# Kernel tuning notes

Hardware: AMD Instinct MI355X
Metric: run time of the kernel (lower is better)

## Reference

```python
import math
import jax, jax.numpy as jnp
import numpy as np

B, S, T = 32, 512, 180
D, F, L, H = 512, 2048, 6, 8
DH = D // H


def _pos_encoding(length, d):
    pos = np.arange(length, dtype=np.float32)[:, None]
    div = np.exp(np.arange(0, d, 2, dtype=np.float32) * (-math.log(10000.0) / d))
    pe = np.zeros((length, d), dtype=np.float32)
    pe[:, 0::2] = np.sin(pos * div)
    pe[:, 1::2] = np.cos(pos * div)
    return jnp.asarray(pe)


def _ln(x, scale, bias):
    mu = x.mean(-1, keepdims=True)
    var = ((x - mu) ** 2).mean(-1, keepdims=True)
    return (x - mu) * jax.lax.rsqrt(var + 1e-5) * scale + bias


def _mha(q_in, kv_in, w, b, causal=False):
    # w: [4, D, D] = (Wq, Wk, Wv, Wo); b: [4, D]
    b_, sq = q_in.shape[:2]
    q = (q_in @ w[0] + b[0]).reshape(b_, sq, H, DH)
    k = (kv_in @ w[1] + b[1]).reshape(b_, -1, H, DH)
    v = (kv_in @ w[2] + b[2]).reshape(b_, -1, H, DH)
    s = jnp.einsum('bqhd,bkhd->bhqk', q, k) / math.sqrt(DH)
    if causal:
        mask = jnp.tril(jnp.ones((sq, k.shape[1]), dtype=bool))
        s = jnp.where(mask, s, -1e9)
    a = jax.nn.softmax(s, axis=-1)
    o = jnp.einsum('bhqk,bkhd->bqhd', a, v).reshape(b_, sq, D)
    return o @ w[3] + b[3]


def _ffn(x, w1, b1, w2, b2):
    return jax.nn.relu(x @ w1 + b1) @ w2 + b2


def setup_inputs() -> dict:
    key = jax.random.key(0)
    ks = jax.random.split(key, 16)
    n = lambda k, shape: jax.random.normal(k, shape, jnp.float32) * 0.02
    return {
        'x': jax.random.normal(ks[0], (B, S, 2), jnp.float32),
        'y_cv_teacher': jax.random.normal(ks[1], (B, T, 1), jnp.float32),
        'src_proj_w': n(ks[2], (2, D)), 'src_proj_b': jnp.zeros((D,), jnp.float32),
        'tgt_proj_w': n(ks[3], (1, D)), 'tgt_proj_b': jnp.zeros((D,), jnp.float32),
        'enc_attn_w': n(ks[4], (L, 4, D, D)), 'enc_attn_b': jnp.zeros((L, 4, D), jnp.float32),
        'enc_ffn_w1': n(ks[5], (L, D, F)), 'enc_ffn_b1': jnp.zeros((L, F), jnp.float32),
        'enc_ffn_w2': n(ks[6], (L, F, D)), 'enc_ffn_b2': jnp.zeros((L, D), jnp.float32),
        'enc_ln_scale': jnp.ones((L, 2, D), jnp.float32), 'enc_ln_bias': jnp.zeros((L, 2, D), jnp.float32),
        'dec_self_w': n(ks[7], (L, 4, D, D)), 'dec_self_b': jnp.zeros((L, 4, D), jnp.float32),
        'dec_cross_w': n(ks[8], (L, 4, D, D)), 'dec_cross_b': jnp.zeros((L, 4, D), jnp.float32),
        'dec_ffn_w1': n(ks[9], (L, D, F)), 'dec_ffn_b1': jnp.zeros((L, F), jnp.float32),
        'dec_ffn_w2': n(ks[10], (L, F, D)), 'dec_ffn_b2': jnp.zeros((L, D), jnp.float32),
        'dec_ln_scale': jnp.ones((L, 3, D), jnp.float32), 'dec_ln_bias': jnp.zeros((L, 3, D), jnp.float32),
        'out_w': n(ks[11], (D, 1)), 'out_b': jnp.zeros((1,), jnp.float32),
    }


def reference(x, y_cv_teacher, src_proj_w, src_proj_b, tgt_proj_w, tgt_proj_b,
              enc_attn_w, enc_attn_b, enc_ffn_w1, enc_ffn_b1, enc_ffn_w2, enc_ffn_b2,
              enc_ln_scale, enc_ln_bias, dec_self_w, dec_self_b, dec_cross_w, dec_cross_b,
              dec_ffn_w1, dec_ffn_b1, dec_ffn_w2, dec_ffn_b2, dec_ln_scale, dec_ln_bias,
              out_w, out_b):
    pe = _pos_encoding(512, D)
    # encoder (post-norm, relu FFN, dropout disabled = eval semantics)
    h = x @ src_proj_w + src_proj_b + pe[: x.shape[1]]
    for i in range(L):
        h = _ln(h + _mha(h, h, enc_attn_w[i], enc_attn_b[i]), enc_ln_scale[i, 0], enc_ln_bias[i, 0])
        h = _ln(h + _ffn(h, enc_ffn_w1[i], enc_ffn_b1[i], enc_ffn_w2[i], enc_ffn_b2[i]),
                enc_ln_scale[i, 1], enc_ln_bias[i, 1])
    memory = h
    # teacher-forced decoder input: [start=0, y_cv_teacher[:-1]]
    tgt_in = jnp.concatenate([jnp.zeros((x.shape[0], 1, 1), x.dtype), y_cv_teacher[:, :-1, :]], axis=1)
    d = tgt_in @ tgt_proj_w + tgt_proj_b + pe[: tgt_in.shape[1]]
    for i in range(L):
        d = _ln(d + _mha(d, d, dec_self_w[i], dec_self_b[i], causal=True),
                dec_ln_scale[i, 0], dec_ln_bias[i, 0])
        d = _ln(d + _mha(d, memory, dec_cross_w[i], dec_cross_b[i]),
                dec_ln_scale[i, 1], dec_ln_bias[i, 1])
        d = _ln(d + _ffn(d, dec_ffn_w1[i], dec_ffn_b1[i], dec_ffn_w2[i], dec_ffn_b2[i]),
                dec_ln_scale[i, 2], dec_ln_bias[i, 2])
    return d @ out_w + out_b  # [B, T, 1]
```

## Files before the change

kernel.cpp:

```cpp
#include <hip/hip_runtime.h>
#include <math.h>

#define B_  32
#define S_  512
#define T_  180
#define D_  512
#define F_  2048
#define L_  6
#define H_  8
#define DH_ 64

typedef unsigned short u16;
typedef __attribute__((ext_vector_type(8))) short short8;
typedef __attribute__((ext_vector_type(4))) float floatx4;

__device__ __forceinline__ float bf2f(u16 h) {
    union { unsigned u; float f; } un; un.u = ((unsigned)h) << 16; return un.f;
}
__device__ __forceinline__ u16 f2bf(float f) {
    union { float f; unsigned u; } un; un.f = f;
    unsigned u = un.u;
    u += 0x7fffu + ((u >> 16) & 1u);
    return (u16)(u >> 16);
}

__device__ __forceinline__ void gload16(const u16* g, u16* l) {
    __builtin_amdgcn_global_load_lds(
        (const __attribute__((address_space(1))) void*)g,
        (__attribute__((address_space(3))) void*)l, 16, 0, 0);
}

__device__ __forceinline__ float pos_enc(int pos, int c) {
    int i2 = c & ~1;
    float div = expf(-(float)i2 * (9.210340371976184f / 512.0f));
    float arg = (float)pos * div;
    return (c & 1) ? cosf(arg) : sinf(arg);
}

__global__ __launch_bounds__(256) void embed_src_kernel(
    const float* __restrict__ x, const float* __restrict__ w,
    const float* __restrict__ b, u16* __restrict__ h)
{
    int idx = blockIdx.x * 256 + threadIdx.x;
    if (idx >= B_ * S_ * D_) return;
    int c  = idx & (D_ - 1);
    int bs = idx >> 9;
    int s  = bs & (S_ - 1);
    float x0 = x[bs * 2 + 0];
    float x1 = x[bs * 2 + 1];
    h[idx] = f2bf(x0 * w[c] + x1 * w[D_ + c] + b[c] + pos_enc(s, c));
}

__global__ __launch_bounds__(256) void embed_tgt_kernel(
    const float* __restrict__ y, const float* __restrict__ w,
    const float* __restrict__ b, u16* __restrict__ d)
{
    int idx = blockIdx.x * 256 + threadIdx.x;
    if (idx >= B_ * T_ * D_) return;
    int c  = idx & (D_ - 1);
    int bt = idx >> 9;
    int t  = bt % T_;
    int bb = bt / T_;
    float tv = (t == 0) ? 0.0f : y[bb * T_ + (t - 1)];
    d[idx] = f2bf(tv * w[c] + b[c] + pos_enc(t, c));
}

__global__ __launch_bounds__(256) void wconv_kernel(
    const float* __restrict__ W, u16* __restrict__ Wt, int K, int N)
{
    __shared__ float tile[32][33];
    size_t mat = (size_t)blockIdx.z * K * N;
    const float* Wm = W + mat;
    u16* Wtm = Wt + mat;
    int n0 = blockIdx.x * 32, k0 = blockIdx.y * 32;
    int tx = threadIdx.x & 31, ty = threadIdx.x >> 5;
#pragma unroll
    for (int i = 0; i < 32; i += 8)
        tile[ty + i][tx] = Wm[(size_t)(k0 + ty + i) * N + n0 + tx];
    __syncthreads();
#pragma unroll
    for (int i = 0; i < 32; i += 8)
        Wtm[(size_t)(n0 + ty + i) * K + k0 + tx] = f2bf(tile[tx][ty + i]);
}

__global__ __launch_bounds__(256) void gemm_bf16_kernel(
    const u16* __restrict__ A, int lda, const u16* __restrict__ Bt,
    const float* __restrict__ bias, u16* __restrict__ C, int ldc,
    int M, int N, int K, int relu)
{
    __shared__ u16 smem[18432];
    u16* As = smem;
    u16* Bs = smem + 8192;

    int tid  = threadIdx.x;
    int w    = tid >> 6;
    int lane = tid & 63;
    int m0 = blockIdx.y << 7, n0 = blockIdx.x << 7;

    int sr = w * 32 + (lane >> 2);
    int sk = (lane & 3) * 8;
    const u16* ag0 = A  + (size_t)(m0 + sr)      * lda + sk;
    const u16* ag1 = A  + (size_t)(m0 + sr + 16) * lda + sk;
    const u16* bg0 = Bt + (size_t)(n0 + sr)      * K + sk;
    const u16* bg1 = Bt + (size_t)(n0 + sr + 16) * K + sk;
    u16* al0 = As + (w * 2 + 0) * 512;
    u16* al1 = As + (w * 2 + 1) * 512;
    u16* bl0 = Bs + (w * 2 + 0) * 512;
    u16* bl1 = Bs + (w * 2 + 1) * 512;

    int wm = (w >> 1) * 64, wn = (w & 1) * 64;
    int fr = lane & 15;
    int fk = (lane >> 4) * 8;

    floatx4 acc[4][4] = {};

    for (int k0 = 0; k0 < K; k0 += 64) {
#pragma unroll
        for (int hh = 0; hh < 2; ++hh) {
            int go = k0 + hh * 32;
            int lo = hh * 4096;
            gload16(ag0 + go, al0 + lo);
            gload16(ag1 + go, al1 + lo);
            gload16(bg0 + go, bl0 + lo);
            gload16(bg1 + go, bl1 + lo);
        }
        __syncthreads();

#pragma unroll
        for (int hh = 0; hh < 2; ++hh) {
            int lo = hh * 4096;
            short8 af[4], bf[4];
#pragma unroll
            for (int i = 0; i < 4; ++i)
                af[i] = *(const short8*)&As[lo + (wm + i * 16 + fr) * 32 + fk];
#pragma unroll
            for (int j = 0; j < 4; ++j)
                bf[j] = *(const short8*)&Bs[lo + (wn + j * 16 + fr) * 32 + fk];
#pragma unroll
            for (int i = 0; i < 4; ++i)
#pragma unroll
                for (int j = 0; j < 4; ++j)
                    acc[i][j] = __builtin_amdgcn_mfma_f32_16x16x32_bf16(
                        af[i], bf[j], acc[i][j], 0, 0, 0);
        }
        __syncthreads();
    }

    u16* epi = smem + w * 4608;
    int cc = lane & 15;
    int rq = (lane >> 4) * 4;
#pragma unroll
    for (int j = 0; j < 4; ++j) {
        float bj = bias[n0 + wn + j * 16 + cc];
#pragma unroll
        for (int i = 0; i < 4; ++i) {
#pragma unroll
            for (int r = 0; r < 4; ++r) {
                float vv = acc[i][j][r] + bj;
                if (relu) vv = fmaxf(vv, 0.f);
                epi[(i * 16 + rq + r) * 72 + j * 16 + cc] = f2bf(vv);
            }
        }
    }
    __syncthreads();
#pragma unroll
    for (int t = 0; t < 8; ++t) {
        int er = t * 8 + (lane >> 3);
        int ec = (lane & 7) * 8;
        short8 vv = *(const short8*)&epi[er * 72 + ec];
        *(short8*)&C[(size_t)(m0 + wm + er) * ldc + n0 + wn + ec] = vv;
    }
}

#define CEXP 0.1803368801111244f

__global__ __launch_bounds__(256) void attn_mfma_kernel(
    const u16* Q, int qs, const u16* __restrict__ K, int ks,
    const u16* __restrict__ V, u16* O,
    int Sq, int Sk, int causal)
{
    __shared__ u16 Qs[64 * 72];
    __shared__ u16 Ks[64 * 72];
    __shared__ u16 Vt[64 * 72];
    __shared__ u16 Ps[4][16 * 72];

    int tid  = threadIdx.x;
    int w    = tid >> 6;
    int lane = tid & 63;
    int n    = lane & 15;
    int quad = lane >> 4;
    int bh = blockIdx.x;
    int bb = bh >> 3, hhd = bh & 7;
    int q0 = blockIdx.y * 64;

    const u16* Qb = Q + (size_t)bb * Sq * qs + hhd * DH_;
    const u16* Kb = K + (size_t)bb * Sk * ks + hhd * DH_;
    const u16* Vb = V + (size_t)bb * Sk * ks + hhd * DH_;

#pragma unroll
    for (int it = 0; it < 2; ++it) {
        int idx = it * 256 + tid;
        int r = idx >> 3, dg = (idx & 7) * 8;
        int qg = q0 + r;
        short8 vv = {};
        if (qg < Sq) vv = *(const short8*)&Qb[(size_t)qg * qs + dg];
        *(short8*)&Qs[r * 72 + dg] = vv;
    }

    float m_i[4], l_i[4];
    floatx4 o_acc[4] = {};
#pragma unroll
    for (int r = 0; r < 4; ++r) { m_i[r] = -1e30f; l_i[r] = 0.f; }

    int qrow0 = q0 + w * 16 + quad * 4;
    int kend = causal ? ((Sk < q0 + 64) ? Sk : (q0 + 64)) : Sk;
    __syncthreads();

    for (int k0 = 0; k0 < kend; k0 += 64) {
#pragma unroll
        for (int it = 0; it < 2; ++it) {
            int idx = it * 256 + tid;
            int r = idx >> 3, dg = (idx & 7) * 8;
            int kg = k0 + r;
            short8 kv = {}, vv = {};
            if (kg < Sk) {
                kv = *(const short8*)&Kb[(size_t)kg * ks + dg];
                vv = *(const short8*)&Vb[(size_t)kg * ks + dg];
            }
            *(short8*)&Ks[r * 72 + dg] = kv;
            int col = (r + dg) & 63;
#pragma unroll
            for (int j = 0; j < 8; ++j)
                Vt[(dg + j) * 72 + col] = (u16)vv[j];
        }
        __syncthreads();

        floatx4 sc[4] = {};
        short8 aq0 = *(const short8*)&Qs[(w * 16 + n) * 72 + quad * 8];
        short8 aq1 = *(const short8*)&Qs[(w * 16 + n) * 72 + 32 + quad * 8];
#pragma unroll
        for (int j = 0; j < 4; ++j) {
            short8 bk0 = *(const short8*)&Ks[(j * 16 + n) * 72 + quad * 8];
            short8 bk1 = *(const short8*)&Ks[(j * 16 + n) * 72 + 32 + quad * 8];
            sc[j] = __builtin_amdgcn_mfma_f32_16x16x32_bf16(aq0, bk0, sc[j], 0, 0, 0);
            sc[j] = __builtin_amdgcn_mfma_f32_16x16x32_bf16(aq1, bk1, sc[j], 0, 0, 0);
        }

        bool need_mask = (k0 + 64 > Sk) ||
                         (causal && (k0 + 63 > q0 + w * 16));
        if (need_mask) {
#pragma unroll
            for (int j = 0; j < 4; ++j) {
                int kg = k0 + j * 16 + n;
#pragma unroll
                for (int r = 0; r < 4; ++r) {
                    if (kg >= Sk || (causal && kg > qrow0 + r))
                        sc[j][r] = -1e30f;
                }
            }
        }

#pragma unroll
        for (int r = 0; r < 4; ++r) {
            float mx = fmaxf(fmaxf(sc[0][r], sc[1][r]), fmaxf(sc[2][r], sc[3][r]));
#pragma unroll
            for (int off = 8; off > 0; off >>= 1)
                mx = fmaxf(mx, __shfl_xor(mx, off, 16));
            float mnew = fmaxf(m_i[r], mx);
            float alpha = exp2f((m_i[r] - mnew) * CEXP);
            m_i[r] = mnew;
            float ps = 0.f;
#pragma unroll
            for (int j = 0; j < 4; ++j) {
                float p = exp2f((sc[j][r] - mnew) * CEXP);
                sc[j][r] = p; ps += p;
            }
#pragma unroll
            for (int off = 8; off > 0; off >>= 1)
                ps += __shfl_xor(ps, off, 16);
            l_i[r] = l_i[r] * alpha + ps;
#pragma unroll
            for (int jb = 0; jb < 4; ++jb) o_acc[jb][r] *= alpha;
        }

#pragma unroll
        for (int j = 0; j < 4; ++j)
#pragma unroll
            for (int r = 0; r < 4; ++r)
                Ps[w][(quad * 4 + r) * 72 + j * 16 + n] = f2bf(sc[j][r]);

        short8 ap0 = *(const short8*)&Ps[w][n * 72 + quad * 8];
        short8 ap1 = *(const short8*)&Ps[w][n * 72 + 32 + quad * 8];
#pragma unroll
        for (int jb = 0; jb < 4; ++jb) {
            int d = jb * 16 + n;
            int rot = d & ~7;
            short8 bv0 = *(const short8*)&Vt[d * 72 + ((quad * 8 + rot) & 63)];
            short8 bv1 = *(const short8*)&Vt[d * 72 + ((32 + quad * 8 + rot) & 63)];
            o_acc[jb] = __builtin_amdgcn_mfma_f32_16x16x32_bf16(ap0, bv0, o_acc[jb], 0, 0, 0);
            o_acc[jb] = __builtin_amdgcn_mfma_f32_16x16x32_bf16(ap1, bv1, o_acc[jb], 0, 0, 0);
        }
        __syncthreads();
    }

    float inv[4];
#pragma unroll
    for (int r = 0; r < 4; ++r) inv[r] = 1.0f / l_i[r];
    u16* Ob = O + (size_t)bb * Sq * qs + hhd * DH_;
#pragma unroll
    for (int r = 0; r < 4; ++r) {
        int qg = qrow0 + r;
        if (qg < Sq) {
#pragma unroll
            for (int jb = 0; jb < 4; ++jb)
                Ob[(size_t)qg * qs + jb * 16 + n] = f2bf(o_acc[jb][r] * inv[r]);
        }
    }
}

__global__ __launch_bounds__(128) void add_ln_kernel(
    u16* __restrict__ h, const u16* __restrict__ delta,
    const float* __restrict__ scale, const float* __restrict__ bias)
{
    __shared__ float red[2][2];
    int row = blockIdx.x, tid = threadIdx.x;
    int lane = tid & 63, wv = tid >> 6;
    size_t base = (size_t)row * D_ + tid * 4;
    uint2 hv = *(const uint2*)&h[base];
    uint2 dv = *(const uint2*)&delta[base];
    float v0 = bf2f(hv.x & 0xffff) + bf2f(dv.x & 0xffff);
    float v1 = bf2f(hv.x >> 16)    + bf2f(dv.x >> 16);
    float v2 = bf2f(hv.y & 0xffff) + bf2f(dv.y & 0xffff);
    float v3 = bf2f(hv.y >> 16)    + bf2f(dv.y >> 16);

    float a  = v0 + v1 + v2 + v3;
    float b2 = v0 * v0 + v1 * v1 + v2 * v2 + v3 * v3;
#pragma unroll
    for (int off = 32; off > 0; off >>= 1) {
        a  += __shfl_xor(a, off);
        b2 += __shfl_xor(b2, off);
    }
    if (lane == 0) { red[wv][0] = a; red[wv][1] = b2; }
    __syncthreads();
    float S1 = red[0][0] + red[1][0];
    float S2 = red[0][1] + red[1][1];
    float mu = S1 * (1.0f / 512.0f);
    float var = S2 * (1.0f / 512.0f) - mu * mu;
    float rs = rsqrtf(var + 1e-5f);

    int c = tid * 4;
    float4 sc = *(const float4*)&scale[c];
    float4 bi = *(const float4*)&bias[c];
    unsigned lo = (unsigned)f2bf((v0 - mu) * rs * sc.x + bi.x) |
                  ((unsigned)f2bf((v1 - mu) * rs * sc.y + bi.y) << 16);
    unsigned hi = (unsigned)f2bf((v2 - mu) * rs * sc.z + bi.z) |
                  ((unsigned)f2bf((v3 - mu) * rs * sc.w + bi.w) << 16);
    *(uint2*)&h[base] = make_uint2(lo, hi);
}

__global__ __launch_bounds__(64) void out_proj_kernel(
    const u16* __restrict__ d, const float* __restrict__ w,
    const float* __restrict__ b, float* __restrict__ out)
{
    int row = blockIdx.x, lane = threadIdx.x;
    float s = 0.f;
    for (int c = lane; c < D_; c += 64) s += bf2f(d[(size_t)row * D_ + c]) * w[c];
#pragma unroll
    for (int off = 32; off > 0; off >>= 1) s += __shfl_down(s, off);
    if (lane == 0) out[row] = s + b[0];
}

extern "C" void kernel_launch(void* const* d_in, const int* in_sizes, int n_in,
                              void* d_out, int out_size, void* d_ws, size_t ws_size,
                              hipStream_t stream)
{
    const float* x          = (const float*)d_in[0];
    const float* y          = (const float*)d_in[1];
    const float* src_w      = (const float*)d_in[2];
    const float* src_b      = (const float*)d_in[3];
    const float* tgt_w      = (const float*)d_in[4];
    const float* tgt_b      = (const float*)d_in[5];
    const float* enc_attn_w = (const float*)d_in[6];
    const float* enc_attn_b = (const float*)d_in[7];
    const float* enc_ffn_w1 = (const float*)d_in[8];
    const float* enc_ffn_b1 = (const float*)d_in[9];
    const float* enc_ffn_w2 = (const float*)d_in[10];
    const float* enc_ffn_b2 = (const float*)d_in[11];
    const float* enc_ln_s   = (const float*)d_in[12];
    const float* enc_ln_b   = (const float*)d_in[13];
    const float* dec_self_w = (const float*)d_in[14];
    const float* dec_self_b = (const float*)d_in[15];
    const float* dec_cross_w= (const float*)d_in[16];
    const float* dec_cross_b= (const float*)d_in[17];
    const float* dec_ffn_w1 = (const float*)d_in[18];
    const float* dec_ffn_b1 = (const float*)d_in[19];
    const float* dec_ffn_w2 = (const float*)d_in[20];
    const float* dec_ffn_b2 = (const float*)d_in[21];
    const float* dec_ln_s   = (const float*)d_in[22];
    const float* dec_ln_b   = (const float*)d_in[23];
    const float* out_w      = (const float*)d_in[24];
    const float* out_b      = (const float*)d_in[25];
    float* out = (float*)d_out;

    const size_t E_BSD = (size_t)B_ * S_ * D_;
    const size_t E_BTD = (size_t)B_ * T_ * D_;
    const size_t WDD   = (size_t)D_ * D_;
    const size_t WDF   = (size_t)D_ * F_;
    const int MS = B_ * S_;
    const int MT = B_ * T_;

    u16* h    = (u16*)d_ws;
    u16* qkv  = h + E_BSD;
    u16* o    = qkv + (size_t)MS * 1536;
    u16* dbuf = o + E_BSD;
    u16* wsc  = dbuf + E_BTD;
    u16* mid  = qkv;
    u16* cq   = qkv;
    u16* ckv  = qkv + 4 * 1024 * 1024;

    auto gemm = [&](const u16* A, int lda, const u16* Wt, const float* bi,
                    u16* C, int ldc, int M, int N, int K, int relu) {
        dim3 g(N / 128, M / 128);
        gemm_bf16_kernel<<<g, dim3(256), 0, stream>>>(A, lda, Wt, bi, C, ldc,
                                                      M, N, K, relu);
    };
    auto attn = [&](const u16* Qp, int qs, const u16* Kp, int ks,
                    const u16* Vp, u16* Op, int Sq, int Sk, int causal) {
        dim3 g(B_ * H_, (Sq + 63) / 64);
        attn_mfma_kernel<<<g, dim3(256), 0, stream>>>(Qp, qs, Kp, ks, Vp, Op,
                                                      Sq, Sk, causal);
    };
    auto addln = [&](u16* hp, const u16* dp, const float* sc, const float* bi,
                     int rows) {
        add_ln_kernel<<<dim3(rows), dim3(128), 0, stream>>>(hp, dp, sc, bi);
    };
    auto wconv = [&](const float* W, u16* Wt, int K, int N, int nmat) {
        wconv_kernel<<<dim3(N / 32, K / 32, nmat), dim3(256), 0, stream>>>(W, Wt, K, N);
    };

    embed_src_kernel<<<dim3((B_ * S_ * D_ + 255) / 256), dim3(256), 0, stream>>>(
        x, src_w, src_b, h);
    for (int l = 0; l < L_; ++l) {
        wconv(enc_attn_w + (size_t)l * 4 * WDD, wsc, D_, D_, 4);
        wconv(enc_ffn_w1 + (size_t)l * WDF, wsc + 4 * WDD, D_, F_, 1);
        wconv(enc_ffn_w2 + (size_t)l * WDF, wsc + 4 * WDD + WDF, F_, D_, 1);

        const float* bl = enc_attn_b + (size_t)l * 4 * D_;
        gemm(h, D_, wsc, bl, qkv, 1536, MS, 1536, D_, 0);
        attn(qkv, 1536, qkv + 512, 1536, qkv + 1024, qkv, S_, S_, 0);
        gemm(qkv, 1536, wsc + 3 * WDD, bl + 3 * D_, o, D_, MS, D_, D_, 0);
        addln(h, o, enc_ln_s + (size_t)l * 2 * D_, enc_ln_b + (size_t)l * 2 * D_, MS);

        for (int m0 = 0; m0 < MS; m0 += 8192) {
            gemm(h + (size_t)m0 * D_, D_, wsc + 4 * WDD,
                 enc_ffn_b1 + (size_t)l * F_, mid, F_, 8192, F_, D_, 1);
            gemm(mid, F_, wsc + 4 * WDD + WDF, enc_ffn_b2 + (size_t)l * D_,
                 o + (size_t)m0 * D_, D_, 8192, D_, F_, 0);
        }
        addln(h, o, enc_ln_s + (size_t)l * 2 * D_ + D_,
              enc_ln_b + (size_t)l * 2 * D_ + D_, MS);
    }

    embed_tgt_kernel<<<dim3((B_ * T_ * D_ + 255) / 256), dim3(256), 0, stream>>>(
        y, tgt_w, tgt_b, dbuf);
    for (int l = 0; l < L_; ++l) {
        wconv(dec_self_w  + (size_t)l * 4 * WDD, wsc, D_, D_, 4);
        wconv(dec_cross_w + (size_t)l * 4 * WDD, wsc + 4 * WDD, D_, D_, 4);
        wconv(dec_ffn_w1  + (size_t)l * WDF, wsc + 8 * WDD, D_, F_, 1);
        wconv(dec_ffn_w2  + (size_t)l * WDF, wsc + 8 * WDD + WDF, F_, D_, 1);

        const float* bl = dec_self_b + (size_t)l * 4 * D_;
        gemm(dbuf, D_, wsc, bl, qkv, 1536, MT, 1536, D_, 0);
        attn(qkv, 1536, qkv + 512, 1536, qkv + 1024, qkv, T_, T_, 1);
        gemm(qkv, 1536, wsc + 3 * WDD, bl + 3 * D_, o, D_, MT, D_, D_, 0);
        addln(dbuf, o, dec_ln_s + (size_t)l * 3 * D_,
              dec_ln_b + (size_t)l * 3 * D_, MT);

        const float* bc = dec_cross_b + (size_t)l * 4 * D_;
        gemm(h, D_, wsc + 5 * WDD, bc + D_, ckv, 1024, MS, 1024, D_, 0);
        gemm(dbuf, D_, wsc + 4 * WDD, bc, cq, D_, MT, D_, D_, 0);
        attn(cq, 512, ckv, 1024, ckv + 512, cq, T_, S_, 0);
        gemm(cq, D_, wsc + 7 * WDD, bc + 3 * D_, o, D_, MT, D_, D_, 0);
        addln(dbuf, o, dec_ln_s + (size_t)l * 3 * D_ + D_,
              dec_ln_b + (size_t)l * 3 * D_ + D_, MT);

        gemm(dbuf, D_, wsc + 8 * WDD, dec_ffn_b1 + (size_t)l * F_,
             mid, F_, MT, F_, D_, 1);
        gemm(mid, F_, wsc + 8 * WDD + WDF, dec_ffn_b2 + (size_t)l * D_,
             o, D_, MT, D_, F_, 0);
        addln(dbuf, o, dec_ln_s + (size_t)l * 3 * D_ + 2 * D_,
              dec_ln_b + (size_t)l * 3 * D_ + 2 * D_, MT);
    }

    out_proj_kernel<<<dim3(MT), dim3(64), 0, stream>>>(dbuf, out_w, out_b, out);
}
```

Baseline: 3.471 ms.

## Add 256x256 tiled, 8-wave pipelined bf16 GEMM for large-M projections

Adds a new GEMM kernel with 256x256 output tiles, 512 threads, swizzled LDS, an XCD-aware block remap and a fine-grained interleaving of global prefetch, LDS reads and MFMA phases gated by explicit barriers and waitcnt. It is used for the encoder QKV projection, the encoder FFN1 and the decoder cross K/V projection. The aim is more data reuse per tile and better overlap of loads with compute. In exchange it uses 128KB of LDS and a large accumulator footprint, so occupancy is low, and it relies on M and N being multiples of 256.

```diff
diff --git a/kernel.cpp b/kernel.cpp
--- a/kernel.cpp
+++ b/kernel.cpp
@@ -169,6 +169,147 @@
         int ec = (lane & 7) * 8;
         short8 vv = *(const short8*)&epi[er * 72 + ec];
         *(short8*)&C[(size_t)(m0 + wm + er) * ldc + n0 + wn + ec] = vv;
+    }
+}
+
+#define SBAR()       asm volatile("s_barrier" ::: "memory")
+#define WAIT_LGKM0() do { asm volatile("s_waitcnt lgkmcnt(0)" ::: "memory"); \
+                          __builtin_amdgcn_sched_barrier(0); } while (0)
+#define WAIT_VM(N)   asm volatile("s_waitcnt vmcnt(" #N ")" ::: "memory")
+
+#define RD_A(BUF, MH) do { \
+  _Pragma("unroll") for (int i_ = 0; i_ < 4; ++i_) \
+  _Pragma("unroll") for (int h_ = 0; h_ < 2; ++h_) \
+    a[i_][h_] = *(const short8*)&smem[(BUF) * 16384 + \
+        ((MH) * 128 + qm + i_ * 16 + fr) * 64 + cSwz[h_]]; \
+} while (0)
+
+#define RD_B(BUF, NH) do { \
+  _Pragma("unroll") for (int n_ = 0; n_ < 2; ++n_) \
+  _Pragma("unroll") for (int h_ = 0; h_ < 2; ++h_) \
+    bb[n_][h_] = *(const short8*)&smem[32768 + (BUF) * 16384 + \
+        ((NH) * 128 + qn + n_ * 16 + fr) * 64 + cSwz[h_]]; \
+} while (0)
+
+#define PH_MMA(MH, NH) do { \
+  __builtin_amdgcn_s_setprio(1); \
+  _Pragma("unroll") for (int i_ = 0; i_ < 4; ++i_) \
+  _Pragma("unroll") for (int n_ = 0; n_ < 2; ++n_) \
+  _Pragma("unroll") for (int h_ = 0; h_ < 2; ++h_) \
+    acc[MH][NH][i_][n_] = __builtin_amdgcn_mfma_f32_16x16x32_bf16( \
+        a[i_][h_], bb[n_][h_], acc[MH][NH][i_][n_], 0, 0, 0); \
+  __builtin_amdgcn_s_setprio(0); \
+} while (0)
+
+__global__ __launch_bounds__(512, 2) void gemm256_bf16_kernel(
+    const u16* __restrict__ A, int lda, const u16* __restrict__ Bt,
+    const float* __restrict__ bias, u16* __restrict__ C, int ldc,
+    int M, int N, int K, int relu)
+{
+    __shared__ __align__(128) u16 smem[65536];
+    const int AB0 = 0, AB1 = 16384, BB0 = 32768, BB1 = 49152;
+
+    int tid = threadIdx.x;
+    int w = tid >> 6, lane = tid & 63;
+    int fr = lane & 15, q = lane >> 4;
+    int qm = (w >> 2) * 64, qn = (w & 3) * 32;
+    int r8 = tid >> 3;
+    int ksrc = (((tid & 7) ^ (r8 & 7)) << 3);
+    int cSwz[2];
+    cSwz[0] = ((q ^ (fr & 7)) << 3);
+    cSwz[1] = (((4 | q) ^ (fr & 7)) << 3);
+
+    int nbx = gridDim.x;
+    int nwg = nbx * gridDim.y;
+    int flat = blockIdx.y * nbx + blockIdx.x;
+    int qq = nwg >> 3, rr = nwg & 7;
+    int xcd = flat & 7, sidx = flat >> 3;
+    int wg = (xcd < rr ? xcd * (qq + 1) : rr * (qq + 1) + (xcd - rr) * qq) + sidx;
+    int m0 = (wg / nbx) << 8, n0 = (wg % nbx) << 8;
+
+    auto stg = [&](const u16* __restrict__ G, int ld, int row0, int bufOff,
+                   int half, int gk) {
+#pragma unroll
+        for (int j = 0; j < 2; ++j) {
+            int rl = half * 128 + j * 64 + r8;
+            gload16(G + (size_t)(row0 + rl) * ld + gk + ksrc,
+                    smem + bufOff + ((half * 128 + j * 64 + (w << 3)) << 6));
+        }
+    };
+
+    short8 a[4][2], bb[2][2];
+    floatx4 acc[2][2][4][2] = {};
+
+    stg(A,  lda, m0, AB0, 0, 0);
+    stg(A,  lda, m0, AB0, 1, 0);
+    stg(Bt, K,   n0, BB0, 0, 0);
+    stg(Bt, K,   n0, BB0, 1, 0);
+    stg(Bt, K,   n0, BB1, 1, 64);
+    stg(A,  lda, m0, AB1, 1, 64);
+    WAIT_VM(0);
+    SBAR();
+
+    int NIT = K >> 7;
+    for (int it = 0; it < NIT; ++it) {
+        const int notlast = (it < NIT - 1);
+        const int gk1 = it * 128 + 64, gk2 = gk1 + 64, gk3 = gk2 + 64;
+        RD_A(0, 0); RD_B(0, 1);
+        stg(A, lda, m0, AB1, 0, gk1);
+        SBAR(); WAIT_LGKM0(); PH_MMA(0, 1); SBAR();
+        RD_A(0, 1);
+        stg(Bt, K, n0, BB1, 0, gk1);
+        SBAR(); WAIT_LGKM0(); PH_MMA(1, 1); SBAR();
+        RD_B(0, 0);
+        if (notlast) stg(Bt, K, n0, BB0, 1, gk2);
+        SBAR(); WAIT_LGKM0(); PH_MMA(1, 0); SBAR();
+        RD_A(0, 0);
+        if (notlast) { stg(A, lda, m0, AB0, 1, gk2); WAIT_VM(4); }
+        else         { WAIT_VM(0); }
+        SBAR(); WAIT_LGKM0(); PH_MMA(0, 0); SBAR();
+        RD_A(1, 0); RD_B(1, 1);
+        if (notlast) stg(A, lda, m0, AB0, 0, gk2);
+        SBAR(); WAIT_LGKM0(); PH_MMA(0, 1); SBAR();
+        RD_A(1, 1);
+        if (notlast) stg(Bt, K, n0, BB0, 0, gk2);
+        SBAR(); WAIT_LGKM0(); PH_MMA(1, 1); SBAR();
+        RD_B(1, 0);
+        if (notlast) stg(Bt, K, n0, BB1, 1, gk3);
+        SBAR(); WAIT_LGKM0(); PH_MMA(1, 0); SBAR();
+        RD_A(1, 0);
+        if (notlast) { stg(A, lda, m0, AB1, 1, gk3); WAIT_VM(4); }
+        SBAR(); WAIT_LGKM0(); PH_MMA(0, 0); SBAR();
+    }
+
+    u16* epi = smem + w * 2560;
+    int rq = q * 4;
+#pragma unroll
+    for (int mh = 0; mh < 2; ++mh) {
+#pragma unroll
+        for (int nh = 0; nh < 2; ++nh) {
+            __syncthreads();
+            int bcol = n0 + nh * 128 + qn;
+            int brow = m0 + mh * 128 + qm;
+#pragma unroll
+            for (int n = 0; n < 2; ++n) {
+                float bj = bias[bcol + n * 16 + fr];
+#pragma unroll
+                for (int i = 0; i < 4; ++i)
+#pragma unroll
+                    for (int r = 0; r < 4; ++r) {
+                        float vv = acc[mh][nh][i][n][r] + bj;
+                        if (relu) vv = fmaxf(vv, 0.f);
+                        epi[(i * 16 + rq + r) * 40 + n * 16 + fr] = f2bf(vv);
+                    }
+            }
+            __syncthreads();
+#pragma unroll
+            for (int t = 0; t < 4; ++t) {
+                int er = t * 16 + (lane >> 2);
+                int ec = (lane & 3) * 8;
+                short8 vv = *(const short8*)&epi[er * 40 + ec];
+                *(short8*)&C[(size_t)(brow + er) * ldc + bcol + ec] = vv;
+            }
+        }
     }
 }
 
@@ -424,6 +565,12 @@
         gemm_bf16_kernel<<<g, dim3(256), 0, stream>>>(A, lda, Wt, bi, C, ldc,
                                                       M, N, K, relu);
     };
+    auto gemm256 = [&](const u16* A, int lda, const u16* Wt, const float* bi,
+                       u16* C, int ldc, int M, int N, int K, int relu) {
+        dim3 g(N / 256, M / 256);
+        gemm256_bf16_kernel<<<g, dim3(512), 0, stream>>>(A, lda, Wt, bi, C, ldc,
+                                                         M, N, K, relu);
+    };
     auto attn = [&](const u16* Qp, int qs, const u16* Kp, int ks,
                     const u16* Vp, u16* Op, int Sq, int Sk, int causal) {
         dim3 g(B_ * H_, (Sq + 63) / 64);
@@ -446,14 +593,14 @@
         wconv(enc_ffn_w2 + (size_t)l * WDF, wsc + 4 * WDD + WDF, F_, D_, 1);
 
         const float* bl = enc_attn_b + (size_t)l * 4 * D_;
-        gemm(h, D_, wsc, bl, qkv, 1536, MS, 1536, D_, 0);
+        gemm256(h, D_, wsc, bl, qkv, 1536, MS, 1536, D_, 0);
         attn(qkv, 1536, qkv + 512, 1536, qkv + 1024, qkv, S_, S_, 0);
         gemm(qkv, 1536, wsc + 3 * WDD, bl + 3 * D_, o, D_, MS, D_, D_, 0);
         addln(h, o, enc_ln_s + (size_t)l * 2 * D_, enc_ln_b + (size_t)l * 2 * D_, MS);
 
         for (int m0 = 0; m0 < MS; m0 += 8192) {
-            gemm(h + (size_t)m0 * D_, D_, wsc + 4 * WDD,
-                 enc_ffn_b1 + (size_t)l * F_, mid, F_, 8192, F_, D_, 1);
+            gemm256(h + (size_t)m0 * D_, D_, wsc + 4 * WDD,
+                    enc_ffn_b1 + (size_t)l * F_, mid, F_, 8192, F_, D_, 1);
             gemm(mid, F_, wsc + 4 * WDD + WDF, enc_ffn_b2 + (size_t)l * D_,
                  o + (size_t)m0 * D_, D_, 8192, D_, F_, 0);
         }
@@ -477,7 +624,7 @@
               dec_ln_b + (size_t)l * 3 * D_, MT);
 
         const float* bc = dec_cross_b + (size_t)l * 4 * D_;
-        gemm(h, D_, wsc + 5 * WDD, bc + D_, ckv, 1024, MS, 1024, D_, 0);
+        gemm256(h, D_, wsc + 5 * WDD, bc + D_, ckv, 1024, MS, 1024, D_, 0);
         gemm(dbuf, D_, wsc + 4 * WDD, bc, cq, D_, MT, D_, D_, 0);
         attn(cq, 512, ckv, 1024, ckv + 512, cq, T_, S_, 0);
         gemm(cq, D_, wsc + 7 * WDD, bc + 3 * D_, o, D_, MT, D_, D_, 0);
```

Result: faster. 3.381 ms (-2.6%).
